# Optimization experiments

Measured on AMD Instinct MI355X. Metric: run time of the kernel, lower is better.

The kernel has to match this reference:

```python
import jax, jax.numpy as jnp
import numpy as np

N_NODES = 50000
N_EDGES = 800000
IN_C, HID_C, OUT_C = 64, 128, 40


def setup_inputs() -> dict:
    key = jax.random.key(0)
    ks = jax.random.split(key, 8)
    x = jax.random.normal(ks[0], (N_NODES, IN_C), dtype=jnp.float32)
    edge_index = jax.random.randint(ks[1], (2, N_EDGES), 0, N_NODES, dtype=jnp.int64)
    def lin(k, fan_in, fan_out):
        # torch Linear default init: U(-1/sqrt(fan_in), 1/sqrt(fan_in))
        bound = 1.0 / np.sqrt(fan_in)
        kw, kb = jax.random.split(k)
        w = jax.random.uniform(kw, (fan_in, fan_out), minval=-bound, maxval=bound, dtype=jnp.float32)
        b = jax.random.uniform(kb, (fan_out,), minval=-bound, maxval=bound, dtype=jnp.float32)
        return w, b
    w1a, b1a = lin(ks[2], IN_C, HID_C)
    w1b, b1b = lin(ks[3], HID_C, HID_C)
    w2a, b2a = lin(ks[4], HID_C, HID_C)
    w2b, b2b = lin(ks[5], HID_C, OUT_C)
    return {
        'x': x, 'edge_index': edge_index,
        'w1a': w1a, 'b1a': b1a, 'w1b': w1b, 'b1b': b1b, 'eps1': jnp.float32(0.0),
        'w2a': w2a, 'b2a': b2a, 'w2b': w2b, 'b2b': b2b, 'eps2': jnp.float32(0.0),
    }


def _gin_conv(x, src, dst, eps, wa, ba, wb, bb):
    # aggregate: sum of neighbor (source) features at each destination node
    agg = jax.ops.segment_sum(x[src], dst, num_segments=N_NODES)  # [N, d]
    h = (1.0 + eps) * x + agg
    h = jax.nn.relu(h @ wa + ba)
    return h @ wb + bb


def reference(x, edge_index, w1a, b1a, w1b, b1b, eps1, w2a, b2a, w2b, b2b, eps2):
    src, dst = edge_index[0], edge_index[1]
    h = _gin_conv(x, src, dst, eps1, w1a, b1a, w1b, b1b)
    h = jax.nn.relu(h)
    # F.dropout(training=False) -> identity at inference
    h = _gin_conv(h, src, dst, eps2, w2a, b2a, w2b, b2b)
    return jax.nn.log_softmax(h, axis=1)
```

## Files before the change

kernel.cpp:

```cpp
#include <hip/hip_runtime.h>
#include <math.h>

#define N_NODES 50000
#define N_EDGES 800000

typedef __attribute__((ext_vector_type(4))) _Float16 half4;
typedef __attribute__((ext_vector_type(8))) _Float16 half8;
typedef __attribute__((ext_vector_type(4))) float f32x4;

__global__ __launch_bounds__(256) void convert_fp16(const float4* __restrict__ in,
    half4* __restrict__ out, int n4)
{
    int i = blockIdx.x * 256 + threadIdx.x;
    if (i >= n4) return;
    float4 v = in[i];
    half4 h;
    h[0] = (_Float16)v.x; h[1] = (_Float16)v.y;
    h[2] = (_Float16)v.z; h[3] = (_Float16)v.w;
    out[i] = h;
}

__global__ __launch_bounds__(256) void scatter_ell(const int* __restrict__ src,
    const int* __restrict__ dst, int* __restrict__ cursor, int* __restrict__ ell)
{
    int e = blockIdx.x * 256 + threadIdx.x;
    if (e >= N_EDGES) return;
    int d = dst[e];
    int slot = atomicAdd(&cursor[d], 1);
    if (slot < 64) ell[(d << 6) + slot] = src[e];
}

__global__ __launch_bounds__(256) void gather64(const half4* __restrict__ rows,
    const int* __restrict__ ell, const int* __restrict__ cursor,
    const float* __restrict__ epsp, half4* __restrict__ z)
{
    const float eps = 1.0f + epsp[0];
    const int lane = threadIdx.x & 63;
    const int q = lane & 15, p = lane >> 4;
    const int wid = blockIdx.x * 4 + (threadIdx.x >> 6);
    const int wstep = gridDim.x * 4;

    for (int node = wid; node < N_NODES; node += wstep) {
        const int cnt = min(cursor[node], 64);
        int eidx = (lane < cnt) ? ell[(node << 6) + lane] : 0;
        float4 acc = make_float4(0.f, 0.f, 0.f, 0.f);
        for (int i = 0; i < cnt; i += 16) {
            int s0 = __shfl(eidx, i + p);
            int s1 = __shfl(eidx, i + 4 + p);
            int s2 = __shfl(eidx, i + 8 + p);
            int s3 = __shfl(eidx, i + 12 + p);
            half4 v0 = rows[s0 * 16 + q];
            half4 v1 = rows[s1 * 16 + q];
            half4 v2 = rows[s2 * 16 + q];
            half4 v3 = rows[s3 * 16 + q];
            bool k0 = (i + p) < cnt, k1 = (i + 4 + p) < cnt;
            bool k2 = (i + 8 + p) < cnt, k3 = (i + 12 + p) < cnt;
            acc.x += (k0?(float)v0[0]:0.f)+(k1?(float)v1[0]:0.f)+(k2?(float)v2[0]:0.f)+(k3?(float)v3[0]:0.f);
            acc.y += (k0?(float)v0[1]:0.f)+(k1?(float)v1[1]:0.f)+(k2?(float)v2[1]:0.f)+(k3?(float)v3[1]:0.f);
            acc.z += (k0?(float)v0[2]:0.f)+(k1?(float)v1[2]:0.f)+(k2?(float)v2[2]:0.f)+(k3?(float)v3[2]:0.f);
            acc.w += (k0?(float)v0[3]:0.f)+(k1?(float)v1[3]:0.f)+(k2?(float)v2[3]:0.f)+(k3?(float)v3[3]:0.f);
        }
        acc.x += __shfl_xor(acc.x, 16); acc.y += __shfl_xor(acc.y, 16);
        acc.z += __shfl_xor(acc.z, 16); acc.w += __shfl_xor(acc.w, 16);
        acc.x += __shfl_xor(acc.x, 32); acc.y += __shfl_xor(acc.y, 32);
        acc.z += __shfl_xor(acc.z, 32); acc.w += __shfl_xor(acc.w, 32);
        if (p == 0) {
            half4 sv = rows[node * 16 + q];
            half4 o;
            o[0] = (_Float16)fmaf(eps, (float)sv[0], acc.x);
            o[1] = (_Float16)fmaf(eps, (float)sv[1], acc.y);
            o[2] = (_Float16)fmaf(eps, (float)sv[2], acc.z);
            o[3] = (_Float16)fmaf(eps, (float)sv[3], acc.w);
            z[node * 16 + q] = o;
        }
    }
}

__global__ __launch_bounds__(256) void gather128(const half4* __restrict__ rows,
    const int* __restrict__ ell, const int* __restrict__ cursor,
    const float* __restrict__ epsp, half4* __restrict__ z)
{
    const float eps = 1.0f + epsp[0];
    const int lane = threadIdx.x & 63;
    const int q = lane & 31, p = lane >> 5;
    const int wid = blockIdx.x * 4 + (threadIdx.x >> 6);
    const int wstep = gridDim.x * 4;

    for (int node = wid; node < N_NODES; node += wstep) {
        const int cnt = min(cursor[node], 64);
        int eidx = (lane < cnt) ? ell[(node << 6) + lane] : 0;
        float4 acc = make_float4(0.f, 0.f, 0.f, 0.f);
        for (int i = 0; i < cnt; i += 8) {
            int s0 = __shfl(eidx, i + p);
            int s1 = __shfl(eidx, i + 2 + p);
            int s2 = __shfl(eidx, i + 4 + p);
            int s3 = __shfl(eidx, i + 6 + p);
            half4 v0 = rows[s0 * 32 + q];
            half4 v1 = rows[s1 * 32 + q];
            half4 v2 = rows[s2 * 32 + q];
            half4 v3 = rows[s3 * 32 + q];
            bool k0 = (i + p) < cnt, k1 = (i + 2 + p) < cnt;
            bool k2 = (i + 4 + p) < cnt, k3 = (i + 6 + p) < cnt;
            acc.x += (k0?(float)v0[0]:0.f)+(k1?(float)v1[0]:0.f)+(k2?(float)v2[0]:0.f)+(k3?(float)v3[0]:0.f);
            acc.y += (k0?(float)v0[1]:0.f)+(k1?(float)v1[1]:0.f)+(k2?(float)v2[1]:0.f)+(k3?(float)v3[1]:0.f);
            acc.z += (k0?(float)v0[2]:0.f)+(k1?(float)v1[2]:0.f)+(k2?(float)v2[2]:0.f)+(k3?(float)v3[2]:0.f);
            acc.w += (k0?(float)v0[3]:0.f)+(k1?(float)v1[3]:0.f)+(k2?(float)v2[3]:0.f)+(k3?(float)v3[3]:0.f);
        }
        acc.x += __shfl_xor(acc.x, 32); acc.y += __shfl_xor(acc.y, 32);
        acc.z += __shfl_xor(acc.z, 32); acc.w += __shfl_xor(acc.w, 32);
        if (p == 0) {
            half4 sv = rows[node * 32 + q];
            half4 o;
            o[0] = (_Float16)fmaf(eps, (float)sv[0], acc.x);
            o[1] = (_Float16)fmaf(eps, (float)sv[1], acc.y);
            o[2] = (_Float16)fmaf(eps, (float)sv[2], acc.z);
            o[3] = (_Float16)fmaf(eps, (float)sv[3], acc.w);
            z[node * 32 + q] = o;
        }
    }
}

template<int K, int N, int EPI>
__global__ __launch_bounds__(512) void gemm_mfma(const _Float16* __restrict__ A,
    const float* __restrict__ W, const float* __restrict__ bias,
    void* __restrict__ Cout, int Nw)
{
    constexpr int S = K / 32, CT = N / 16;
    extern __shared__ half8 frag[];
    const int tid = threadIdx.x;

    for (int idx = tid; idx < S * CT * 64; idx += 512) {
        int l = idx & 63, f = idx >> 6;
        int s = f / CT, ct = f % CT;
        int c = ct * 16 + (l & 15);
        int k0 = s * 32 + (l >> 4) * 8;
        half8 hi, lo;
        #pragma unroll
        for (int i = 0; i < 8; ++i) {
            float w = (c < Nw) ? W[(k0 + i) * Nw + c] : 0.0f;
            _Float16 h = (_Float16)w;
            hi[i] = h;
            lo[i] = (_Float16)(w - (float)h);
        }
        frag[(f * 2 + 0) * 64 + l] = hi;
        frag[(f * 2 + 1) * 64 + l] = lo;
    }
    __syncthreads();

    const int lane = tid & 63;
    const int g = lane >> 4;
    const int tile = blockIdx.x * 8 + (tid >> 6);
    if (tile >= N_NODES / 16) return;

    float bl[CT];
    #pragma unroll
    for (int ct = 0; ct < CT; ++ct) {
        int c = ct * 16 + (lane & 15);
        bl[ct] = (c < Nw) ? bias[c] : 0.0f;
    }

    const _Float16* Ar = A + (size_t)(tile * 16 + (lane & 15)) * K;
    f32x4 acc[CT];
    #pragma unroll
    for (int ct = 0; ct < CT; ++ct) acc[ct] = (f32x4){0.f, 0.f, 0.f, 0.f};

    #pragma unroll
    for (int s = 0; s < S; ++s) {
        half8 a = *(const half8*)(Ar + s * 32 + g * 8);
        #pragma unroll
        for (int ct = 0; ct < CT; ++ct) {
            half8 bh = frag[((s * CT + ct) * 2 + 0) * 64 + lane];
            half8 bo = frag[((s * CT + ct) * 2 + 1) * 64 + lane];
            acc[ct] = __builtin_amdgcn_mfma_f32_16x16x32_f16(a, bh, acc[ct], 0, 0, 0);
            acc[ct] = __builtin_amdgcn_mfma_f32_16x16x32_f16(a, bo, acc[ct], 0, 0, 0);
        }
    }

    if (EPI == 0) {
        _Float16* C = (_Float16*)Cout;
        #pragma unroll
        for (int r = 0; r < 4; ++r) {
            int row = tile * 16 + g * 4 + r;
            #pragma unroll
            for (int ct = 0; ct < CT; ++ct) {
                float v = fmaxf(acc[ct][r] + bl[ct], 0.0f);
                C[(size_t)row * N + ct * 16 + (lane & 15)] = (_Float16)v;
            }
        }
    } else {
        float* C = (float*)Cout;
        const bool va2 = (lane & 15) < 8;
        #pragma unroll
        for (int r = 0; r < 4; ++r) {
            int row = tile * 16 + g * 4 + r;
            float v0 = acc[0][r] + bl[0];
            float v1 = acc[1][r] + bl[1];
            float v2 = acc[2][r] + bl[2];
            float mx = fmaxf(fmaxf(v0, v1), va2 ? v2 : -__builtin_inff());
            mx = fmaxf(mx, __shfl_xor(mx, 1));
            mx = fmaxf(mx, __shfl_xor(mx, 2));
            mx = fmaxf(mx, __shfl_xor(mx, 4));
            mx = fmaxf(mx, __shfl_xor(mx, 8));
            float sm = expf(v0 - mx) + expf(v1 - mx) + (va2 ? expf(v2 - mx) : 0.f);
            sm += __shfl_xor(sm, 1);
            sm += __shfl_xor(sm, 2);
            sm += __shfl_xor(sm, 4);
            sm += __shfl_xor(sm, 8);
            float ls = logf(sm) + mx;
            C[row * 40 + (lane & 15)] = v0 - ls;
            C[row * 40 + 16 + (lane & 15)] = v1 - ls;
            if (va2) C[row * 40 + 32 + (lane & 15)] = v2 - ls;
        }
    }
}

extern "C" void kernel_launch(void* const* d_in, const int* in_sizes, int n_in,
                              void* d_out, int out_size, void* d_ws, size_t ws_size,
                              hipStream_t stream) {
    const float* x    = (const float*)d_in[0];
    const int*   ei   = (const int*)d_in[1];
    const float* w1a  = (const float*)d_in[2];
    const float* b1a  = (const float*)d_in[3];
    const float* w1b  = (const float*)d_in[4];
    const float* b1b  = (const float*)d_in[5];
    const float* eps1 = (const float*)d_in[6];
    const float* w2a  = (const float*)d_in[7];
    const float* b2a  = (const float*)d_in[8];
    const float* w2b  = (const float*)d_in[9];
    const float* b2b  = (const float*)d_in[10];
    const float* eps2 = (const float*)d_in[11];
    float* out = (float*)d_out;

    const int* srcIdx = ei;
    const int* dstIdx = ei + N_EDGES;

    char* ws = (char*)d_ws;
    int*      cursor = (int*)(ws);
    int*      ell    = (int*)(ws + 262144);
    _Float16* xh     = (_Float16*)(ws + 13200000);
    _Float16* z1h    = (_Float16*)(ws + 19700000);
    _Float16* mid1h  = (_Float16*)(ws + 26200000);
    _Float16* h1h    = (_Float16*)(ws + 39100000);
    _Float16* z2h    = (_Float16*)(ws + 52000000);
    _Float16* mid2h  = (_Float16*)(ws + 64900000);

    hipMemsetAsync(cursor, 0, 200000, stream);

    convert_fp16<<<3125, 256, 0, stream>>>((const float4*)x, (half4*)xh, 800000);
    scatter_ell<<<3125, 256, 0, stream>>>(srcIdx, dstIdx, cursor, ell);

    gather64<<<2048, 256, 0, stream>>>((const half4*)xh, ell, cursor, eps1, (half4*)z1h);
    gemm_mfma<64, 128, 0><<<391, 512, 32768, stream>>>(z1h, w1a, b1a, mid1h, 128);
    gemm_mfma<128, 128, 0><<<391, 512, 65536, stream>>>(mid1h, w1b, b1b, h1h, 128);
    gather128<<<2048, 256, 0, stream>>>((const half4*)h1h, ell, cursor, eps2, (half4*)z2h);
    gemm_mfma<128, 128, 0><<<391, 512, 65536, stream>>>(z2h, w2a, b2a, mid2h, 128);
    gemm_mfma<128, 48, 1><<<391, 512, 24576, stream>>>(mid2h, w2b, b2b, out, 40);
}
```

Baseline: 223.0 us.

## Fuse GIN MLP GEMM pairs and build a 16-bit ELL via partitioned scatter

Each GIN layer's two linear layers now run in one kernel, with the hidden tile kept in swizzled shared memory, so the mid activations never make a round trip through global memory. Adjacency construction splits edges into 8 groups with per-group cursors plus an overflow list, then compacts them into a 16-bit ELL with degree counts. This spreads atomic contention and halves index bandwidth in the gathers. Zeroing of the cursors is folded into the conversion kernel, replacing the memset. The costs are more shared memory per block (limiting occupancy), an extra compaction pass, and a possible drop of edges when a node's overflow exceeds its caps.

```diff
diff --git a/kernel.cpp b/kernel.cpp
--- a/kernel.cpp
+++ b/kernel.cpp
@@ -8,30 +8,64 @@
 typedef __attribute__((ext_vector_type(8))) _Float16 half8;
 typedef __attribute__((ext_vector_type(4))) float f32x4;
 
-__global__ __launch_bounds__(256) void convert_fp16(const float4* __restrict__ in,
-    half4* __restrict__ out, int n4)
+__global__ __launch_bounds__(256) void convert_zero(const float4* __restrict__ in,
+    half4* __restrict__ out, int* __restrict__ zbase)
 {
     int i = blockIdx.x * 256 + threadIdx.x;
-    if (i >= n4) return;
-    float4 v = in[i];
-    half4 h;
-    h[0] = (_Float16)v.x; h[1] = (_Float16)v.y;
-    h[2] = (_Float16)v.z; h[3] = (_Float16)v.w;
-    out[i] = h;
+    if (i < 450000) zbase[i] = 0;
+    if (i < 800000) {
+        float4 v = in[i];
+        half4 h;
+        h[0] = (_Float16)v.x; h[1] = (_Float16)v.y;
+        h[2] = (_Float16)v.z; h[3] = (_Float16)v.w;
+        out[i] = h;
+    }
 }
 
 __global__ __launch_bounds__(256) void scatter_ell(const int* __restrict__ src,
-    const int* __restrict__ dst, int* __restrict__ cursor, int* __restrict__ ell)
-{
-    int e = blockIdx.x * 256 + threadIdx.x;
-    if (e >= N_EDGES) return;
+    const int* __restrict__ dst, int* __restrict__ cursor8, int* __restrict__ ovcur,
+    unsigned short* __restrict__ ellp, unsigned short* __restrict__ ovell)
+{
+    int g = blockIdx.x & 7;
+    int el = (blockIdx.x >> 3) * 256 + threadIdx.x;
+    if (el >= 100000) return;
+    int e = g * 100000 + el;
     int d = dst[e];
-    int slot = atomicAdd(&cursor[d], 1);
-    if (slot < 64) ell[(d << 6) + slot] = src[e];
+    unsigned short s = (unsigned short)src[e];
+    int slot = atomicAdd(&cursor8[g * 50000 + d], 1);
+    if (slot < 8) ellp[(size_t)(g * 50000 + d) * 8 + slot] = s;
+    else {
+        int o = atomicAdd(&ovcur[d], 1);
+        if (o < 16) ovell[d * 16 + o] = s;
+    }
+}
+
+__global__ __launch_bounds__(256) void compact_ell(const int* __restrict__ cursor8,
+    const int* __restrict__ ovcur, const unsigned short* __restrict__ ellp,
+    const unsigned short* __restrict__ ovell,
+    unsigned short* __restrict__ ell, int* __restrict__ deg)
+{
+    __shared__ unsigned short buf[4][80];
+    const int w = threadIdx.x >> 6, lane = threadIdx.x & 63;
+    const int node = blockIdx.x * 4 + w;
+    const int g = lane >> 3, sl = lane & 7;
+    int cg = min(cursor8[g * 50000 + node], 8);
+    bool valid = sl < cg;
+    unsigned short v = ellp[(size_t)(g * 50000 + node) * 8 + sl];
+    unsigned long long mask = __ballot(valid);
+    int total = __popcll(mask);
+    int pos = __popcll(mask & ((1ULL << lane) - 1ULL));
+    if (valid) buf[w][pos] = v;
+    int ov = min(ovcur[node], 16);
+    if (lane < ov) buf[w][total + lane] = ovell[node * 16 + lane];
+    __syncthreads();
+    int tot = min(total + ov, 64);
+    ell[((size_t)node << 6) + lane] = (lane < tot) ? buf[w][lane] : (unsigned short)0;
+    if (lane == 0) deg[node] = tot;
 }
 
 __global__ __launch_bounds__(256) void gather64(const half4* __restrict__ rows,
-    const int* __restrict__ ell, const int* __restrict__ cursor,
+    const unsigned short* __restrict__ ell, const int* __restrict__ deg,
     const float* __restrict__ epsp, half4* __restrict__ z)
 {
     const float eps = 1.0f + epsp[0];
@@ -41,8 +75,8 @@
     const int wstep = gridDim.x * 4;
 
     for (int node = wid; node < N_NODES; node += wstep) {
-        const int cnt = min(cursor[node], 64);
-        int eidx = (lane < cnt) ? ell[(node << 6) + lane] : 0;
+        const int cnt = min(deg[node], 64);
+        int eidx = (lane < cnt) ? ell[((size_t)node << 6) + lane] : 0;
         float4 acc = make_float4(0.f, 0.f, 0.f, 0.f);
         for (int i = 0; i < cnt; i += 16) {
             int s0 = __shfl(eidx, i + p);
@@ -77,7 +111,7 @@
 }
 
 __global__ __launch_bounds__(256) void gather128(const half4* __restrict__ rows,
-    const int* __restrict__ ell, const int* __restrict__ cursor,
+    const unsigned short* __restrict__ ell, const int* __restrict__ deg,
     const float* __restrict__ epsp, half4* __restrict__ z)
 {
     const float eps = 1.0f + epsp[0];
@@ -87,8 +121,8 @@
     const int wstep = gridDim.x * 4;
 
     for (int node = wid; node < N_NODES; node += wstep) {
-        const int cnt = min(cursor[node], 64);
-        int eidx = (lane < cnt) ? ell[(node << 6) + lane] : 0;
+        const int cnt = min(deg[node], 64);
+        int eidx = (lane < cnt) ? ell[((size_t)node << 6) + lane] : 0;
         float4 acc = make_float4(0.f, 0.f, 0.f, 0.f);
         for (int i = 0; i < cnt; i += 8) {
             int s0 = __shfl(eidx, i + p);
@@ -120,82 +154,131 @@
     }
 }
 
-template<int K, int N, int EPI>
-__global__ __launch_bounds__(512) void gemm_mfma(const _Float16* __restrict__ A,
-    const float* __restrict__ W, const float* __restrict__ bias,
-    void* __restrict__ Cout, int Nw)
-{
-    constexpr int S = K / 32, CT = N / 16;
-    extern __shared__ half8 frag[];
+template<int KA, int NB, int EPI>
+__global__ __launch_bounds__(512) void fused_mlp(const _Float16* __restrict__ A,
+    const float* __restrict__ wA, const float* __restrict__ bA,
+    const float* __restrict__ wB, const float* __restrict__ bB,
+    void* __restrict__ Cout, int NwB)
+{
+    constexpr int SA = KA / 32, CTB = NB / 16;
+    extern __shared__ char smem[];
+    half8* fragA = (half8*)smem;
+    half8* fragB = (half8*)(smem + SA * 8 * 2 * 64 * 16);
+    char* midbase = smem + SA * 8 * 2 * 64 * 16 + 4 * CTB * 2 * 64 * 16;
     const int tid = threadIdx.x;
 
-    for (int idx = tid; idx < S * CT * 64; idx += 512) {
+    for (int idx = tid; idx < SA * 8 * 64; idx += 512) {
         int l = idx & 63, f = idx >> 6;
-        int s = f / CT, ct = f % CT;
+        int s = f >> 3, ct = f & 7;
         int c = ct * 16 + (l & 15);
         int k0 = s * 32 + (l >> 4) * 8;
         half8 hi, lo;
         #pragma unroll
         for (int i = 0; i < 8; ++i) {
-            float w = (c < Nw) ? W[(k0 + i) * Nw + c] : 0.0f;
-            _Float16 h = (_Float16)w;
+            float wv = wA[(k0 + i) * 128 + c];
+            _Float16 h = (_Float16)wv;
             hi[i] = h;
-            lo[i] = (_Float16)(w - (float)h);
-        }
-        frag[(f * 2 + 0) * 64 + l] = hi;
-        frag[(f * 2 + 1) * 64 + l] = lo;
+            lo[i] = (_Float16)(wv - (float)h);
+        }
+        fragA[(f * 2 + 0) * 64 + l] = hi;
+        fragA[(f * 2 + 1) * 64 + l] = lo;
+    }
+    for (int idx = tid; idx < 4 * CTB * 64; idx += 512) {
+        int l = idx & 63, f = idx >> 6;
+        int s = f / CTB, ct = f % CTB;
+        int c = ct * 16 + (l & 15);
+        int k0 = s * 32 + (l >> 4) * 8;
+        half8 hi, lo;
+        #pragma unroll
+        for (int i = 0; i < 8; ++i) {
+            float wv = (c < NwB) ? wB[(k0 + i) * NwB + c] : 0.0f;
+            _Float16 h = (_Float16)wv;
+            hi[i] = h;
+            lo[i] = (_Float16)(wv - (float)h);
+        }
+        fragB[(f * 2 + 0) * 64 + l] = hi;
+        fragB[(f * 2 + 1) * 64 + l] = lo;
     }
     __syncthreads();
 
     const int lane = tid & 63;
-    const int g = lane >> 4;
+    const int gg = lane >> 4, r16 = lane & 15;
     const int tile = blockIdx.x * 8 + (tid >> 6);
     if (tile >= N_NODES / 16) return;
-
-    float bl[CT];
-    #pragma unroll
-    for (int ct = 0; ct < CT; ++ct) {
-        int c = ct * 16 + (lane & 15);
-        bl[ct] = (c < Nw) ? bias[c] : 0.0f;
-    }
-
-    const _Float16* Ar = A + (size_t)(tile * 16 + (lane & 15)) * K;
-    f32x4 acc[CT];
-    #pragma unroll
-    for (int ct = 0; ct < CT; ++ct) acc[ct] = (f32x4){0.f, 0.f, 0.f, 0.f};
-
-    #pragma unroll
-    for (int s = 0; s < S; ++s) {
-        half8 a = *(const half8*)(Ar + s * 32 + g * 8);
-        #pragma unroll
-        for (int ct = 0; ct < CT; ++ct) {
-            half8 bh = frag[((s * CT + ct) * 2 + 0) * 64 + lane];
-            half8 bo = frag[((s * CT + ct) * 2 + 1) * 64 + lane];
+    char* my = midbase + (tid >> 6) * 4096;
+
+    const _Float16* Ar = A + (size_t)(tile * 16 + r16) * KA;
+    f32x4 acc[8];
+    #pragma unroll
+    for (int ct = 0; ct < 8; ++ct) acc[ct] = (f32x4){0.f, 0.f, 0.f, 0.f};
+    #pragma unroll
+    for (int s = 0; s < SA; ++s) {
+        half8 a = *(const half8*)(Ar + s * 32 + gg * 8);
+        #pragma unroll
+        for (int ct = 0; ct < 8; ++ct) {
+            half8 bh = fragA[((s * 8 + ct) * 2 + 0) * 64 + lane];
+            half8 bo = fragA[((s * 8 + ct) * 2 + 1) * 64 + lane];
             acc[ct] = __builtin_amdgcn_mfma_f32_16x16x32_f16(a, bh, acc[ct], 0, 0, 0);
             acc[ct] = __builtin_amdgcn_mfma_f32_16x16x32_f16(a, bo, acc[ct], 0, 0, 0);
         }
     }
+    #pragma unroll
+    for (int ct = 0; ct < 8; ++ct) {
+        float bb = bA[ct * 16 + r16];
+        #pragma unroll
+        for (int r = 0; r < 4; ++r) {
+            int row = gg * 4 + r;
+            float v = fmaxf(acc[ct][r] + bb, 0.0f);
+            int off = (row << 8) + ((ct * 16 + r16) << 1);
+            off ^= (row & 7) << 4;
+            *(_Float16*)(my + off) = (_Float16)v;
+        }
+    }
+
+    half8 a2[4];
+    #pragma unroll
+    for (int s = 0; s < 4; ++s) {
+        int off = (r16 << 8) + (s << 6) + (gg << 4);
+        off ^= (r16 & 7) << 4;
+        a2[s] = *(const half8*)(my + off);
+    }
+    f32x4 acc2[CTB];
+    #pragma unroll
+    for (int ct = 0; ct < CTB; ++ct) acc2[ct] = (f32x4){0.f, 0.f, 0.f, 0.f};
+    #pragma unroll
+    for (int s = 0; s < 4; ++s) {
+        #pragma unroll
+        for (int ct = 0; ct < CTB; ++ct) {
+            half8 bh = fragB[((s * CTB + ct) * 2 + 0) * 64 + lane];
+            half8 bo = fragB[((s * CTB + ct) * 2 + 1) * 64 + lane];
+            acc2[ct] = __builtin_amdgcn_mfma_f32_16x16x32_f16(a2[s], bh, acc2[ct], 0, 0, 0);
+            acc2[ct] = __builtin_amdgcn_mfma_f32_16x16x32_f16(a2[s], bo, acc2[ct], 0, 0, 0);
+        }
+    }
 
     if (EPI == 0) {
         _Float16* C = (_Float16*)Cout;
         #pragma unroll
-        for (int r = 0; r < 4; ++r) {
-            int row = tile * 16 + g * 4 + r;
+        for (int ct = 0; ct < CTB; ++ct) {
+            float bb = bB[ct * 16 + r16];
             #pragma unroll
-            for (int ct = 0; ct < CT; ++ct) {
-                float v = fmaxf(acc[ct][r] + bl[ct], 0.0f);
-                C[(size_t)row * N + ct * 16 + (lane & 15)] = (_Float16)v;
+            for (int r = 0; r < 4; ++r) {
+                int row = tile * 16 + gg * 4 + r;
+                float v = fmaxf(acc2[ct][r] + bb, 0.0f);
+                C[(size_t)row * NB + ct * 16 + r16] = (_Float16)v;
             }
         }
     } else {
         float* C = (float*)Cout;
-        const bool va2 = (lane & 15) < 8;
+        const bool va2 = r16 < 8;
+        float bl0 = bB[r16], bl1 = bB[16 + r16];
+        float bl2 = va2 ? bB[32 + r16] : 0.0f;
         #pragma unroll
         for (int r = 0; r < 4; ++r) {
-            int row = tile * 16 + g * 4 + r;
-            float v0 = acc[0][r] + bl[0];
-            float v1 = acc[1][r] + bl[1];
-            float v2 = acc[2][r] + bl[2];
+            int row = tile * 16 + gg * 4 + r;
+            float v0 = acc2[0][r] + bl0;
+            float v1 = acc2[1][r] + bl1;
+            float v2 = acc2[2][r] + bl2;
             float mx = fmaxf(fmaxf(v0, v1), va2 ? v2 : -__builtin_inff());
             mx = fmaxf(mx, __shfl_xor(mx, 1));
             mx = fmaxf(mx, __shfl_xor(mx, 2));
@@ -207,9 +290,9 @@
             sm += __shfl_xor(sm, 4);
             sm += __shfl_xor(sm, 8);
             float ls = logf(sm) + mx;
-            C[row * 40 + (lane & 15)] = v0 - ls;
-            C[row * 40 + 16 + (lane & 15)] = v1 - ls;
-            if (va2) C[row * 40 + 32 + (lane & 15)] = v2 - ls;
+            C[row * 40 + r16] = v0 - ls;
+            C[row * 40 + 16 + r16] = v1 - ls;
+            if (va2) C[row * 40 + 32 + r16] = v2 - ls;
         }
     }
 }
@@ -235,24 +318,23 @@
     const int* dstIdx = ei + N_EDGES;
 
     char* ws = (char*)d_ws;
-    int*      cursor = (int*)(ws);
-    int*      ell    = (int*)(ws + 262144);
-    _Float16* xh     = (_Float16*)(ws + 13200000);
-    _Float16* z1h    = (_Float16*)(ws + 19700000);
-    _Float16* mid1h  = (_Float16*)(ws + 26200000);
-    _Float16* h1h    = (_Float16*)(ws + 39100000);
-    _Float16* z2h    = (_Float16*)(ws + 52000000);
-    _Float16* mid2h  = (_Float16*)(ws + 64900000);
-
-    hipMemsetAsync(cursor, 0, 200000, stream);
-
-    convert_fp16<<<3125, 256, 0, stream>>>((const float4*)x, (half4*)xh, 800000);
-    scatter_ell<<<3125, 256, 0, stream>>>(srcIdx, dstIdx, cursor, ell);
-
-    gather64<<<2048, 256, 0, stream>>>((const half4*)xh, ell, cursor, eps1, (half4*)z1h);
-    gemm_mfma<64, 128, 0><<<391, 512, 32768, stream>>>(z1h, w1a, b1a, mid1h, 128);
-    gemm_mfma<128, 128, 0><<<391, 512, 65536, stream>>>(mid1h, w1b, b1b, h1h, 128);
-    gather128<<<2048, 256, 0, stream>>>((const half4*)h1h, ell, cursor, eps2, (half4*)z2h);
-    gemm_mfma<128, 128, 0><<<391, 512, 65536, stream>>>(z2h, w2a, b2a, mid2h, 128);
-    gemm_mfma<128, 48, 1><<<391, 512, 24576, stream>>>(mid2h, w2b, b2b, out, 40);
-}
+    int*            cursor8 = (int*)(ws);
+    int*            ovcur   = (int*)(ws + 1600000);
+    unsigned short* ellp    = (unsigned short*)(ws + 1800000);
+    unsigned short* ovell   = (unsigned short*)(ws + 8200000);
+    unsigned short* ell     = (unsigned short*)(ws + 9800000);
+    int*            deg     = (int*)(ws + 16200000);
+    _Float16*       xh      = (_Float16*)(ws + 16400000);
+    _Float16*       z1h     = (_Float16*)(ws + 22800000);
+    _Float16*       h1h     = (_Float16*)(ws + 29200000);
+    _Float16*       z2h     = (_Float16*)(ws + 42000000);
+
+    convert_zero<<<3125, 256, 0, stream>>>((const float4*)x, (half4*)xh, cursor8);
+    scatter_ell<<<3128, 256, 0, stream>>>(srcIdx, dstIdx, cursor8, ovcur, ellp, ovell);
+    compact_ell<<<12500, 256, 0, stream>>>(cursor8, ovcur, ellp, ovell, ell, deg);
+
+    gather64<<<2048, 256, 0, stream>>>((const half4*)xh, ell, deg, eps1, (half4*)z1h);
+    fused_mlp<64, 128, 0><<<391, 512, 131072, stream>>>(z1h, w1a, b1a, w1b, b1b, h1h, 128);
+    gather128<<<2048, 256, 0, stream>>>((const half4*)h1h, ell, deg, eps2, (half4*)z2h);
+    fused_mlp<128, 48, 1><<<391, 512, 122880, stream>>>(z2h, w2a, b2a, w2b, b2b, out, 40);
+}
```

New measurement: 215.4 us. -3.4%, faster.
